# Optimization experiments

Measured on AMD Instinct MI355X. Metric: run time of the kernel, lower is better.

The kernel has to match this reference:

```python
import jax, jax.numpy as jnp
import numpy as np

B, C, H, W = 8, 64, 64, 64
CQ = C // 8  # query/key channels


def setup_inputs() -> dict:
    key = jax.random.key(0)
    ks = jax.random.split(key, 7)
    s = 0.05
    return {
        "x": jax.random.normal(ks[0], (B, C, H, W), jnp.float32),
        "wq": jax.random.normal(ks[1], (CQ, C), jnp.float32) * s,
        "bq": jnp.zeros((CQ,), jnp.float32),
        "wk": jax.random.normal(ks[2], (CQ, C), jnp.float32) * s,
        "bk": jnp.zeros((CQ,), jnp.float32),
        "wv": jax.random.normal(ks[3], (C, C), jnp.float32) * s,
        "bv": jnp.zeros((C,), jnp.float32),
    }


def reference(x, wq, bq, wk, bk, wv, bv):
    b, c, h, w = x.shape
    n = h * w
    xf = x.reshape(b, c, n)                       # [B, C, N]
    # 1x1 convs == per-pixel linear over channels
    q = jnp.einsum('oc,bcn->bon', wq, xf) + bq[None, :, None]   # [B, CQ, N]
    k = jnp.einsum('oc,bcn->bon', wk, xf) + bk[None, :, None]   # [B, CQ, N]
    v = jnp.einsum('oc,bcn->bon', wv, xf) + bv[None, :, None]   # [B, C, N]
    # energy[b, i, j] = q[b, :, i] . k[b, :, j]  (unscaled)
    energy = jnp.einsum('bci,bcj->bij', q, k)     # [B, N, N]
    attention = jax.nn.softmax(energy, axis=-1)   # softmax over j
    # out[b, c, i] = sum_j v[b, c, j] * attention[b, i, j]
    out = jnp.einsum('bcj,bij->bci', v, attention)
    return out.reshape(b, c, h, w)
```

## Files before the change

kernel.cpp:

```cpp
#include <hip/hip_runtime.h>
#include <hip/hip_bf16.h>


#define B_   8
#define C_   64
#define N_   4096
#define LOG2E 1.44269504088896340736f

typedef short bf16x8 __attribute__((ext_vector_type(8)));
typedef float f32x4  __attribute__((ext_vector_type(4)));
typedef unsigned int uint32;

#if __has_builtin(__builtin_amdgcn_exp2f)
#define EXP2(x) __builtin_amdgcn_exp2f(x)
#else
#define EXP2(x) __expf((x) * 0.69314718055994530942f)
#endif

__device__ __forceinline__ unsigned short f2bf_rn(float f) {
    union { __hip_bfloat16 h; unsigned short u; } cv;
    cv.h = __float2bfloat16(f);
    return cv.u;
}
__device__ __forceinline__ uint32 pk_rn(float lo, float hi) {
    return (uint32)f2bf_rn(lo) | ((uint32)f2bf_rn(hi) << 16);
}
__device__ __forceinline__ uint32 pack_rtz(float lo, float hi) {
    return __builtin_amdgcn_perm(__float_as_uint(hi), __float_as_uint(lo), 0x07060302);
}

__global__ __launch_bounds__(256) void prep_kernel(
    const float* __restrict__ x,
    const float* __restrict__ wq, const float* __restrict__ bq,
    const float* __restrict__ wk, const float* __restrict__ bk,
    unsigned short* __restrict__ Qh, unsigned short* __restrict__ Kh,
    unsigned short* __restrict__ Xb)
{
    __shared__ float Xs[C_][64];
    __shared__ float Wqk[16][C_];
    __shared__ float Bqk[16];

    const int t  = threadIdx.x;
    const int b  = blockIdx.x >> 6;
    const int p0 = (blockIdx.x & 63) << 6;

    for (int i = t; i < 1024; i += 256) {
        int o = i >> 6;
        Wqk[o][i & 63] = (o < 8) ? wq[i] * LOG2E : wk[i - 512];
    }
    if (t < 16) Bqk[t] = (t < 8) ? bq[t] * LOG2E : bk[t - 8];

    for (int i = t; i < 2048; i += 256) {
        int c = i >> 5, p2 = (i & 31) << 1;
        const float* xp = x + ((size_t)b * C_ + c) * N_ + p0 + p2;
        float2 v = *(const float2*)xp;
        Xs[c][p2] = v.x; Xs[c][p2 + 1] = v.y;
        *(uint32*)(Xb + ((size_t)b * C_ + c) * N_ + p0 + p2) = pk_rn(v.x, v.y);
    }
    __syncthreads();

    const int pix = t & 63, grp = t >> 6;
    float a[4];
    #pragma unroll
    for (int r = 0; r < 4; ++r) a[r] = Bqk[grp * 4 + r];
    for (int c = 0; c < C_; ++c) {
        float xv = Xs[c][pix];
        #pragma unroll
        for (int r = 0; r < 4; ++r) a[r] += Wqk[grp * 4 + r][c] * xv;
    }
    #pragma unroll
    for (int r = 0; r < 4; ++r) {
        int o = grp * 4 + r;
        unsigned short hv = f2bf_rn(a[r]);
        if (o < 8) Qh[((size_t)b * N_ + p0 + pix) * 8 + o] = hv;
        else       Kh[((size_t)b * N_ + p0 + pix) * 8 + (o - 8)] = hv;
    }
}

__global__ __launch_bounds__(512) void attn_mfma7_kernel(
    const unsigned short* __restrict__ Qh,
    const unsigned short* __restrict__ Kh,
    const unsigned short* __restrict__ Xb,
    const float* __restrict__ wv, const float* __restrict__ bv,
    float* __restrict__ out)
{
    __shared__ __align__(16) char smem[67584];

    const int t    = threadIdx.x;
    const int w    = t >> 6;
    const int lane = t & 63;
    const int l16  = lane & 15;
    const int qd   = lane >> 4;
    const int b    = blockIdx.x >> 6;
    const int i0   = (blockIdx.x & 63) << 6;

    const bf16x8 z8 = {};
    const f32x4  zf = {};

    bf16x8 qf[4];
    #pragma unroll
    for (int qt = 0; qt < 4; ++qt) {
        qf[qt] = z8;
        if (qd == 0)
            qf[qt] = *(const bf16x8*)(Qh + ((size_t)b * N_ + i0 + qt * 16 + l16) * 8);
    }

    const unsigned short* Kp = Kh + ((size_t)b * N_ + w * 512) * 8;
    const unsigned short* Xp = Xb + (size_t)b * C_ * N_ + w * 512;

    f32x4 acc[4][4];
    #pragma unroll
    for (int ct = 0; ct < 4; ++ct)
        #pragma unroll
        for (int qt = 0; qt < 4; ++qt) acc[ct][qt] = zf;
    float dsum[4] = {0.f, 0.f, 0.f, 0.f};

    const int swz   = (l16 & 3) << 2;
    const int wbase = w * 4096 + l16 * 64;
    int woff[2];
    #pragma unroll
    for (int jt = 0; jt < 2; ++jt) woff[jt] = ((jt * 8 + qd * 2) ^ swz) << 2;
    const int roff = ((qd * 4) ^ swz) << 2;

    bf16x8 kf[2][2], xf[2][4];
    #pragma unroll
    for (int jt = 0; jt < 2; ++jt) {
        kf[0][jt] = z8;
        if (qd == 0) kf[0][jt] = *(const bf16x8*)(Kp + (jt * 16 + l16) * 8);
    }
    #pragma unroll
    for (int ct = 0; ct < 4; ++ct)
        xf[0][ct] = *(const bf16x8*)(Xp + (size_t)(ct * 16 + l16) * N_ + qd * 8);

    #pragma unroll 2
    for (int s = 0; s < 16; ++s) {
        const int cur = s & 1, nxt = cur ^ 1;
        const int jb = s * 32;

        f32x4 sf[2][4];
        #pragma unroll
        for (int jt = 0; jt < 2; ++jt)
            #pragma unroll
            for (int qt = 0; qt < 4; ++qt)
                sf[jt][qt] = __builtin_amdgcn_mfma_f32_16x16x32_bf16(kf[cur][jt], qf[qt], zf, 0, 0, 0);

        if (s < 15) {
            #pragma unroll
            for (int jt = 0; jt < 2; ++jt) {
                bf16x8 nk = z8;
                if (qd == 0) nk = *(const bf16x8*)(Kp + (size_t)(jb + 32 + jt * 16 + l16) * 8);
                kf[nxt][jt] = nk;
            }
            #pragma unroll
            for (int ct = 0; ct < 4; ++ct)
                xf[nxt][ct] = *(const bf16x8*)(Xp + (size_t)(ct * 16 + l16) * N_ + jb + 32 + qd * 8);
        }

        #pragma unroll
        for (int jt = 0; jt < 2; ++jt)
            #pragma unroll
            for (int qt = 0; qt < 4; ++qt) {
                float e0 = EXP2(sf[jt][qt][0]);
                float e1 = EXP2(sf[jt][qt][1]);
                float e2 = EXP2(sf[jt][qt][2]);
                float e3 = EXP2(sf[jt][qt][3]);
                dsum[qt] += (e0 + e1) + (e2 + e3);
                uint2 u;
                u.x = pack_rtz(e0, e1);
                u.y = pack_rtz(e2, e3);
                *(uint2*)(smem + wbase + qt * 1024 + woff[jt]) = u;
            }

        #pragma unroll
        for (int qt = 0; qt < 4; ++qt) {
            bf16x8 pb = *(const bf16x8*)(smem + wbase + qt * 1024 + roff);
            #pragma unroll
            for (int ct = 0; ct < 4; ++ct)
                acc[ct][qt] = __builtin_amdgcn_mfma_f32_16x16x32_bf16(xf[cur][ct], pb, acc[ct][qt], 0, 0, 0);
        }
    }

    #pragma unroll
    for (int qt = 0; qt < 4; ++qt) {
        float v = dsum[qt];
        v += __shfl_xor(v, 16, 64);
        v += __shfl_xor(v, 32, 64);
        if (qd == 0) *(float*)(smem + 65536 + (w * 64 + qt * 16 + l16) * 4) = v;
    }

    __syncthreads();
    if (w >= 4) {
        char* rb = smem + (w - 4) * 16384;
        #pragma unroll
        for (int ct = 0; ct < 4; ++ct)
            #pragma unroll
            for (int qt = 0; qt < 4; ++qt)
                *(f32x4*)(rb + (ct * 4 + qt) * 1024 + lane * 16) = acc[ct][qt];
    }
    __syncthreads();
    if (w < 4) {
        const char* rb = smem + w * 16384;
        #pragma unroll
        for (int ct = 0; ct < 4; ++ct)
            #pragma unroll
            for (int qt = 0; qt < 4; ++qt)
                acc[ct][qt] += *(const f32x4*)(rb + (ct * 4 + qt) * 1024 + lane * 16);
    }
    __syncthreads();
    if (w >= 1 && w < 4) {
        char* rb = smem + w * 16384;
        #pragma unroll
        for (int ct = 0; ct < 4; ++ct)
            #pragma unroll
            for (int qt = 0; qt < 4; ++qt)
                *(f32x4*)(rb + (ct * 4 + qt) * 1024 + lane * 16) = acc[ct][qt];
    }
    if (w >= 4) {
        float* Wvs = (float*)smem;
        for (int i = t - 256; i < 4096; i += 256) Wvs[i] = wv[i];
    }
    __syncthreads();
    if (w == 0) {
        #pragma unroll
        for (int rr = 1; rr < 4; ++rr)
            #pragma unroll
            for (int ct = 0; ct < 4; ++ct)
                #pragma unroll
                for (int qt = 0; qt < 4; ++qt) {
                    f32x4 p = *(const f32x4*)(smem + rr * 16384 + (ct * 4 + qt) * 1024 + lane * 16);
                    acc[ct][qt] += p;
                }
        float* Or = (float*)(smem + 16384);
        #pragma unroll
        for (int ct = 0; ct < 4; ++ct)
            #pragma unroll
            for (int qt = 0; qt < 4; ++qt)
                #pragma unroll
                for (int r = 0; r < 4; ++r)
                    Or[(ct * 16 + qd * 4 + r) * 64 + qt * 16 + l16] = acc[ct][qt][r];
    }
    __syncthreads();

    const int q = t & 63, grp = t >> 6;
    const float* Wvs = (const float*)smem;
    const float* Or  = (const float*)(smem + 16384);
    const float* Dn  = (const float*)(smem + 65536);
    float dtot = 0.f;
    #pragma unroll
    for (int r = 0; r < 8; ++r) dtot += Dn[r * 64 + q];
    const float inv = 1.0f / dtot;
    float o[8];
    #pragma unroll
    for (int r = 0; r < 8; ++r) o[r] = 0.f;
    for (int k = 0; k < 64; ++k) {
        float ov = Or[k * 64 + q];
        #pragma unroll
        for (int r = 0; r < 8; ++r)
            o[r] += Wvs[(grp * 8 + r) * 64 + k] * ov;
    }
    #pragma unroll
    for (int r = 0; r < 8; ++r)
        out[((size_t)b * C_ + grp * 8 + r) * N_ + i0 + q] = o[r] * inv + bv[grp * 8 + r];
}

__global__ __launch_bounds__(256) void attn_fused_fallback(
    const float* __restrict__ x,
    const float* __restrict__ wq, const float* __restrict__ bq,
    const float* __restrict__ wk, const float* __restrict__ bk,
    const float* __restrict__ wv, const float* __restrict__ bv,
    float* __restrict__ out)
{
    __shared__ float Qs[64][8];
    __shared__ float Ks[8][64];
    __shared__ float Vs[64][C_];
    __shared__ float Ws[64][64 + 1];
    __shared__ float Xs[C_ * 64];
    __shared__ float Wks[8][C_];
    __shared__ float Wvs[C_][C_ + 1];

    const int t     = threadIdx.x;
    const int b     = blockIdx.x / (N_ / 64);
    const int i0    = (blockIdx.x % (N_ / 64)) * 64;
    const int jlane = t & 63;
    const int wgrp  = t >> 6;

    for (int l = t; l < 8 * C_;  l += 256) Wks[l >> 6][l & 63] = wk[l];
    for (int l = t; l < C_ * C_; l += 256) Wvs[l >> 6][l & 63] = wv[l];
    for (int l = t; l < C_ * 64; l += 256)
        Xs[(l >> 6) * 64 + (l & 63)] = x[((size_t)b * C_ + (l >> 6)) * N_ + i0 + (l & 63)];
    __syncthreads();
    {
        int qi = jlane;
        #pragma unroll
        for (int r = 0; r < 2; ++r) {
            int cc = wgrp * 2 + r;
            float a = bq[cc];
            for (int c = 0; c < C_; ++c) a += wq[cc * C_ + c] * Xs[c * 64 + qi];
            Qs[qi][cc] = a;
        }
    }
    __syncthreads();

    const int qi2 = t >> 2;
    const int cb  = (t & 3) << 4;
    float accv[16];
    #pragma unroll
    for (int r = 0; r < 16; ++r) accv[r] = 0.f;
    float denom = 0.f;

    for (int j0 = 0; j0 < N_; j0 += 64) {
        for (int l = t; l < C_ * 64; l += 256)
            Xs[(l >> 6) * 64 + (l & 63)] = x[((size_t)b * C_ + (l >> 6)) * N_ + j0 + (l & 63)];
        __syncthreads();
        {
            int j = jlane;
            #pragma unroll
            for (int r = 0; r < 2; ++r) {
                int cc = wgrp * 2 + r;
                float a = bk[cc];
                for (int c = 0; c < C_; ++c) a += Wks[cc][c] * Xs[c * 64 + j];
                Ks[cc][j] = a;
            }
        }
        {
            int vc = jlane;
            #pragma unroll 2
            for (int r = 0; r < 16; ++r) {
                int j = wgrp * 16 + r;
                float a = bv[vc];
                for (int c = 0; c < C_; ++c) a += Wvs[vc][c] * Xs[c * 64 + j];
                Vs[j][vc] = a;
            }
        }
        __syncthreads();
        {
            float kreg[8];
            #pragma unroll
            for (int cc = 0; cc < 8; ++cc) kreg[cc] = Ks[cc][jlane];
            #pragma unroll 4
            for (int r = 0; r < 16; ++r) {
                int qi = wgrp * 16 + r;
                float e = 0.f;
                #pragma unroll
                for (int cc = 0; cc < 8; ++cc) e += Qs[qi][cc] * kreg[cc];
                Ws[qi][jlane] = __expf(e);
            }
        }
        __syncthreads();
        #pragma unroll 4
        for (int j = 0; j < 64; ++j) {
            float wv2 = Ws[qi2][j];
            denom += wv2;
            const float4* vrow = (const float4*)(&Vs[j][cb]);
            float4 v0 = vrow[0], v1 = vrow[1], v2 = vrow[2], v3 = vrow[3];
            accv[0]  += wv2 * v0.x; accv[1]  += wv2 * v0.y; accv[2]  += wv2 * v0.z; accv[3]  += wv2 * v0.w;
            accv[4]  += wv2 * v1.x; accv[5]  += wv2 * v1.y; accv[6]  += wv2 * v1.z; accv[7]  += wv2 * v1.w;
            accv[8]  += wv2 * v2.x; accv[9]  += wv2 * v2.y; accv[10] += wv2 * v2.z; accv[11] += wv2 * v2.w;
            accv[12] += wv2 * v3.x; accv[13] += wv2 * v3.y; accv[14] += wv2 * v3.z; accv[15] += wv2 * v3.w;
        }
        __syncthreads();
    }

    const float inv = 1.0f / denom;
    #pragma unroll
    for (int r = 0; r < 16; ++r)
        out[((size_t)b * C_ + cb + r) * N_ + i0 + qi2] = accv[r] * inv;
}

extern "C" void kernel_launch(void* const* d_in, const int* in_sizes, int n_in,
                              void* d_out, int out_size, void* d_ws, size_t ws_size,
                              hipStream_t stream)
{
    const float* x  = (const float*)d_in[0];
    const float* wq = (const float*)d_in[1];
    const float* bq = (const float*)d_in[2];
    const float* wk = (const float*)d_in[3];
    const float* bk = (const float*)d_in[4];
    const float* wv = (const float*)d_in[5];
    const float* bv = (const float*)d_in[6];
    float* out = (float*)d_out;

    const size_t nQ = (size_t)B_ * N_ * 8;
    const size_t nX = (size_t)B_ * C_ * N_;
    const size_t needed = (2 * nQ + nX) * sizeof(unsigned short);

    if (ws_size >= needed) {
        unsigned short* Qh = (unsigned short*)d_ws;
        unsigned short* Kh = Qh + nQ;
        unsigned short* Xb = Kh + nQ;
        prep_kernel<<<B_ * (N_ / 64), 256, 0, stream>>>(x, wq, bq, wk, bk, Qh, Kh, Xb);
        attn_mfma7_kernel<<<B_ * (N_ / 64), 512, 0, stream>>>(Qh, Kh, Xb, wv, bv, out);
    } else {
        attn_fused_fallback<<<B_ * (N_ / 64), 256, 0, stream>>>(x, wq, bq, wk, bk, wv, bv, out);
    }
}
```

Before: 132.0 us.

## Split waves across key partitions and channel halves with a shared P tile

```diff
diff --git a/kernel.cpp b/kernel.cpp
--- a/kernel.cpp
+++ b/kernel.cpp
@@ -77,7 +77,7 @@
     }
 }
 
-__global__ __launch_bounds__(512) void attn_mfma7_kernel(
+__global__ __launch_bounds__(512, 4) void attn_mfma9_kernel(
     const unsigned short* __restrict__ Qh,
     const unsigned short* __restrict__ Kh,
     const unsigned short* __restrict__ Xb,
@@ -91,6 +91,8 @@
     const int lane = t & 63;
     const int l16  = lane & 15;
     const int qd   = lane >> 4;
+    const int p    = w & 3;
+    const int h    = w >> 2;
     const int b    = blockIdx.x >> 6;
     const int i0   = (blockIdx.x & 63) << 6;
 
@@ -105,78 +107,69 @@
             qf[qt] = *(const bf16x8*)(Qh + ((size_t)b * N_ + i0 + qt * 16 + l16) * 8);
     }
 
-    const unsigned short* Kp = Kh + ((size_t)b * N_ + w * 512) * 8;
-    const unsigned short* Xp = Xb + (size_t)b * C_ * N_ + w * 512;
-
-    f32x4 acc[4][4];
-    #pragma unroll
-    for (int ct = 0; ct < 4; ++ct)
+    const unsigned short* Kp = Kh + ((size_t)b * N_ + p * 1024 + h * 16) * 8;
+    const unsigned short* Xp = Xb + ((size_t)b * C_ + h * 32) * N_ + p * 1024;
+
+    f32x4 acc[2][4];
+    #pragma unroll
+    for (int ct = 0; ct < 2; ++ct)
         #pragma unroll
         for (int qt = 0; qt < 4; ++qt) acc[ct][qt] = zf;
     float dsum[4] = {0.f, 0.f, 0.f, 0.f};
 
     const int swz   = (l16 & 3) << 2;
-    const int wbase = w * 4096 + l16 * 64;
-    int woff[2];
-    #pragma unroll
-    for (int jt = 0; jt < 2; ++jt) woff[jt] = ((jt * 8 + qd * 2) ^ swz) << 2;
-    const int roff = ((qd * 4) ^ swz) << 2;
-
-    bf16x8 kf[2][2], xf[2][4];
-    #pragma unroll
-    for (int jt = 0; jt < 2; ++jt) {
-        kf[0][jt] = z8;
-        if (qd == 0) kf[0][jt] = *(const bf16x8*)(Kp + (jt * 16 + l16) * 8);
-    }
-    #pragma unroll
-    for (int ct = 0; ct < 4; ++ct)
+    const int pbase = p * 8192 + l16 * 64;
+    const int woff  = ((h * 8 + qd * 2) ^ swz) << 2;
+    const int roff  = ((qd * 4) ^ swz) << 2;
+
+    bf16x8 kf[2], xf[2][2];
+    kf[0] = z8;
+    if (qd == 0) kf[0] = *(const bf16x8*)(Kp + (size_t)l16 * 8);
+    #pragma unroll
+    for (int ct = 0; ct < 2; ++ct)
         xf[0][ct] = *(const bf16x8*)(Xp + (size_t)(ct * 16 + l16) * N_ + qd * 8);
 
     #pragma unroll 2
-    for (int s = 0; s < 16; ++s) {
+    for (int s = 0; s < 32; ++s) {
         const int cur = s & 1, nxt = cur ^ 1;
         const int jb = s * 32;
-
-        f32x4 sf[2][4];
-        #pragma unroll
-        for (int jt = 0; jt < 2; ++jt)
-            #pragma unroll
-            for (int qt = 0; qt < 4; ++qt)
-                sf[jt][qt] = __builtin_amdgcn_mfma_f32_16x16x32_bf16(kf[cur][jt], qf[qt], zf, 0, 0, 0);
-
-        if (s < 15) {
-            #pragma unroll
-            for (int jt = 0; jt < 2; ++jt) {
-                bf16x8 nk = z8;
-                if (qd == 0) nk = *(const bf16x8*)(Kp + (size_t)(jb + 32 + jt * 16 + l16) * 8);
-                kf[nxt][jt] = nk;
-            }
-            #pragma unroll
-            for (int ct = 0; ct < 4; ++ct)
+        char* pb_ = smem + pbase + cur * 4096;
+
+        f32x4 sf[4];
+        #pragma unroll
+        for (int qt = 0; qt < 4; ++qt)
+            sf[qt] = __builtin_amdgcn_mfma_f32_16x16x32_bf16(kf[cur], qf[qt], zf, 0, 0, 0);
+
+        if (s < 31) {
+            bf16x8 nk = z8;
+            if (qd == 0) nk = *(const bf16x8*)(Kp + (size_t)(jb + 32 + l16) * 8);
+            kf[nxt] = nk;
+            #pragma unroll
+            for (int ct = 0; ct < 2; ++ct)
                 xf[nxt][ct] = *(const bf16x8*)(Xp + (size_t)(ct * 16 + l16) * N_ + jb + 32 + qd * 8);
         }
 
         #pragma unroll
-        for (int jt = 0; jt < 2; ++jt)
-            #pragma unroll
-            for (int qt = 0; qt < 4; ++qt) {
-                float e0 = EXP2(sf[jt][qt][0]);
-                float e1 = EXP2(sf[jt][qt][1]);
-                float e2 = EXP2(sf[jt][qt][2]);
-                float e3 = EXP2(sf[jt][qt][3]);
-                dsum[qt] += (e0 + e1) + (e2 + e3);
-                uint2 u;
-                u.x = pack_rtz(e0, e1);
-                u.y = pack_rtz(e2, e3);
-                *(uint2*)(smem + wbase + qt * 1024 + woff[jt]) = u;
-            }
-
-        #pragma unroll
         for (int qt = 0; qt < 4; ++qt) {
-            bf16x8 pb = *(const bf16x8*)(smem + wbase + qt * 1024 + roff);
-            #pragma unroll
-            for (int ct = 0; ct < 4; ++ct)
-                acc[ct][qt] = __builtin_amdgcn_mfma_f32_16x16x32_bf16(xf[cur][ct], pb, acc[ct][qt], 0, 0, 0);
+            float e0 = EXP2(sf[qt][0]);
+            float e1 = EXP2(sf[qt][1]);
+            float e2 = EXP2(sf[qt][2]);
+            float e3 = EXP2(sf[qt][3]);
+            dsum[qt] += (e0 + e1) + (e2 + e3);
+            uint2 u;
+            u.x = pack_rtz(e0, e1);
+            u.y = pack_rtz(e2, e3);
+            *(uint2*)(pb_ + qt * 1024 + woff) = u;
+        }
+
+        __syncthreads();
+
+        #pragma unroll
+        for (int qt = 0; qt < 4; ++qt) {
+            bf16x8 pbf = *(const bf16x8*)(pb_ + qt * 1024 + roff);
+            #pragma unroll
+            for (int ct = 0; ct < 2; ++ct)
+                acc[ct][qt] = __builtin_amdgcn_mfma_f32_16x16x32_bf16(xf[cur][ct], pbf, acc[ct][qt], 0, 0, 0);
         }
     }
 
@@ -189,61 +182,45 @@
     }
 
     __syncthreads();
-    if (w >= 4) {
-        char* rb = smem + (w - 4) * 16384;
-        #pragma unroll
-        for (int ct = 0; ct < 4; ++ct)
+    if (p != 0) {
+        const int slot = h * 3 + (p - 1);
+        char* rb = smem + slot * 8192;
+        #pragma unroll
+        for (int ct = 0; ct < 2; ++ct)
             #pragma unroll
             for (int qt = 0; qt < 4; ++qt)
                 *(f32x4*)(rb + (ct * 4 + qt) * 1024 + lane * 16) = acc[ct][qt];
     }
     __syncthreads();
-    if (w < 4) {
-        const char* rb = smem + w * 16384;
-        #pragma unroll
-        for (int ct = 0; ct < 4; ++ct)
-            #pragma unroll
-            for (int qt = 0; qt < 4; ++qt)
-                acc[ct][qt] += *(const f32x4*)(rb + (ct * 4 + qt) * 1024 + lane * 16);
-    }
-    __syncthreads();
-    if (w >= 1 && w < 4) {
-        char* rb = smem + w * 16384;
-        #pragma unroll
-        for (int ct = 0; ct < 4; ++ct)
-            #pragma unroll
-            for (int qt = 0; qt < 4; ++qt)
-                *(f32x4*)(rb + (ct * 4 + qt) * 1024 + lane * 16) = acc[ct][qt];
-    }
-    if (w >= 4) {
-        float* Wvs = (float*)smem;
-        for (int i = t - 256; i < 4096; i += 256) Wvs[i] = wv[i];
-    }
-    __syncthreads();
-    if (w == 0) {
-        #pragma unroll
-        for (int rr = 1; rr < 4; ++rr)
-            #pragma unroll
-            for (int ct = 0; ct < 4; ++ct)
+    if (p == 0) {
+        #pragma unroll
+        for (int rr = 0; rr < 3; ++rr) {
+            const char* rb = smem + (h * 3 + rr) * 8192;
+            #pragma unroll
+            for (int ct = 0; ct < 2; ++ct)
                 #pragma unroll
-                for (int qt = 0; qt < 4; ++qt) {
-                    f32x4 p = *(const f32x4*)(smem + rr * 16384 + (ct * 4 + qt) * 1024 + lane * 16);
-                    acc[ct][qt] += p;
-                }
-        float* Or = (float*)(smem + 16384);
-        #pragma unroll
-        for (int ct = 0; ct < 4; ++ct)
+                for (int qt = 0; qt < 4; ++qt)
+                    acc[ct][qt] += *(const f32x4*)(rb + (ct * 4 + qt) * 1024 + lane * 16);
+        }
+        float* Or = (float*)(smem + 49152);
+        #pragma unroll
+        for (int ct = 0; ct < 2; ++ct)
             #pragma unroll
             for (int qt = 0; qt < 4; ++qt)
                 #pragma unroll
                 for (int r = 0; r < 4; ++r)
-                    Or[(ct * 16 + qd * 4 + r) * 64 + qt * 16 + l16] = acc[ct][qt][r];
+                    Or[(h * 32 + ct * 16 + qd * 4 + r) * 64 + qt * 16 + l16] = acc[ct][qt][r];
+    }
+    __syncthreads();
+    {
+        float* Wvs = (float*)smem;
+        for (int i = t; i < 4096; i += 512) Wvs[i] = wv[i];
     }
     __syncthreads();
 
     const int q = t & 63, grp = t >> 6;
     const float* Wvs = (const float*)smem;
-    const float* Or  = (const float*)(smem + 16384);
+    const float* Or  = (const float*)(smem + 49152);
     const float* Dn  = (const float*)(smem + 65536);
     float dtot = 0.f;
     #pragma unroll
@@ -389,7 +366,7 @@
         unsigned short* Kh = Qh + nQ;
         unsigned short* Xb = Kh + nQ;
         prep_kernel<<<B_ * (N_ / 64), 256, 0, stream>>>(x, wq, bq, wk, bk, Qh, Kh, Xb);
-        attn_mfma7_kernel<<<B_ * (N_ / 64), 512, 0, stream>>>(Qh, Kh, Xb, wv, bv, out);
+        attn_mfma9_kernel<<<B_ * (N_ / 64), 512, 0, stream>>>(Qh, Kh, Xb, wv, bv, out);
     } else {
         attn_fused_fallback<<<B_ * (N_ / 64), 256, 0, stream>>>(x, wq, bq, wk, bk, wv, bv, out);
     }
```

New measurement: 123.9 us. -6.2%, faster.
